# Kernel optimization log

Measured on AMD Instinct MI355X. Metric: run time of the kernel, lower is better.

## Reference

```python
import jax, jax.numpy as jnp
import numpy as np

N_SRC0, N_DST0 = 200000, 40000
N_SRC1, N_DST1 = 40000, 8000
E0, E1 = 1000000, 80000
D_IN, D_HID, D_OUT = 256, 512, 256


def setup_inputs() -> dict:
    key = jax.random.key(0)
    ks = jax.random.split(key, 10)
    return {
        "feat": jax.random.normal(ks[0], (N_SRC0, D_IN), dtype=jnp.float32),
        "Wself0": jax.random.normal(ks[1], (D_IN, D_HID), dtype=jnp.float32) * 0.05,
        "Wneigh0": jax.random.normal(ks[2], (D_IN, D_HID), dtype=jnp.float32) * 0.05,
        "b0": jnp.zeros((D_HID,), dtype=jnp.float32),
        "Wself1": jax.random.normal(ks[3], (D_HID, D_OUT), dtype=jnp.float32) * 0.05,
        "Wneigh1": jax.random.normal(ks[4], (D_HID, D_OUT), dtype=jnp.float32) * 0.05,
        "b1": jnp.zeros((D_OUT,), dtype=jnp.float32),
        "edge_src0": jax.random.randint(ks[5], (E0,), 0, N_SRC0, dtype=jnp.int32),
        "edge_dst0": jax.random.randint(ks[6], (E0,), 0, N_DST0, dtype=jnp.int32),
        "edge_src1": jax.random.randint(ks[7], (E1,), 0, N_SRC1, dtype=jnp.int32),
        "edge_dst1": jax.random.randint(ks[8], (E1,), 0, N_DST1, dtype=jnp.int32),
    }


def _mean_agg(h_src, src, dst, n_dst):
    # gather src features along edges, segment-mean over dst nodes
    msg_sum = jax.ops.segment_sum(h_src[src], dst, num_segments=n_dst)  # [n_dst, d]
    deg = jax.ops.segment_sum(jnp.ones(dst.shape, h_src.dtype), dst, num_segments=n_dst)
    return msg_sum / jnp.maximum(deg, 1.0)[:, None]


def _sage_layer(h, src, dst, n_dst, W_self, W_neigh, b):
    # DGL SAGEConv(mean): fc_self(h_dst) + fc_neigh(mean_neighbors) + bias
    h_dst = h[:n_dst]
    h_neigh = _mean_agg(h, src, dst, n_dst)
    return h_dst @ W_self + h_neigh @ W_neigh + b


def reference(feat, Wself0, Wneigh0, b0, Wself1, Wneigh1, b1,
              edge_src0, edge_dst0, edge_src1, edge_dst1):
    h = _sage_layer(feat, edge_src0, edge_dst0, N_DST0, Wself0, Wneigh0, b0)
    h = jax.nn.relu(h)  # ReLU between layers, not after last
    h = _sage_layer(h, edge_src1, edge_dst1, N_DST1, Wself1, Wneigh1, b1)
    return h
```

## Files before the change

### kernel.cpp

```cpp
#include <hip/hip_runtime.h>

#define DEV __device__ __forceinline__

typedef float f32x4 __attribute__((ext_vector_type(4)));
typedef short s16x4 __attribute__((ext_vector_type(4)));
typedef short s16x8 __attribute__((ext_vector_type(8)));

DEV float bf2f(short s) {
  unsigned u = ((unsigned)(unsigned short)s) << 16;
  return __builtin_bit_cast(float, u);
}
DEV short f2bf(float f) {
  unsigned u = __builtin_bit_cast(unsigned, f);
  u += 0x7FFFu + ((u >> 16) & 1u);
  return (short)(u >> 16);
}

DEV void gld_lds16(const void* g, void* l) {
  __builtin_amdgcn_global_load_lds(
      (const __attribute__((address_space(1))) void*)g,
      (__attribute__((address_space(3))) void*)l, 16, 0, 0);
}

__global__ void front_k(const float* __restrict__ feat, short* __restrict__ fbf, long nconv,
                        const float* __restrict__ Ws0, const float* __restrict__ Wn0,
                        short* __restrict__ W0T,
                        const float* __restrict__ Ws1, const float* __restrict__ Wn1,
                        short* __restrict__ W1T,
                        const int* __restrict__ es0, const int* __restrict__ ed0, int E0,
                        int* __restrict__ cnt0, int* __restrict__ bk0,
                        const int* __restrict__ es1, const int* __restrict__ ed1, int E1,
                        int* __restrict__ cnt1, int* __restrict__ bk1) {
  const int b = blockIdx.x, tid = threadIdx.x;
  if (b < 1664) {
    long i = ((long)b * 256 + tid) * 8;
    const long stride = (long)1664 * 256 * 8;
    for (; i < nconv; i += stride) {
      f32x4 v0 = *(const f32x4*)(feat + i);
      f32x4 v1 = *(const f32x4*)(feat + i + 4);
      s16x8 o;
      o[0] = f2bf(v0[0]); o[1] = f2bf(v0[1]); o[2] = f2bf(v0[2]); o[3] = f2bf(v0[3]);
      o[4] = f2bf(v1[0]); o[5] = f2bf(v1[1]); o[6] = f2bf(v1[2]); o[7] = f2bf(v1[3]);
      *(s16x8*)(fbf + i) = o;
    }
  } else if (b < 1728) {
    for (int idx = (b - 1664) * 256 + tid; idx < 524288; idx += 64 * 256) {
      if (idx < 262144) {
        int n = idx >> 9, k = idx & 511;
        float v = (k < 256) ? Ws0[(size_t)k * 512 + n] : Wn0[(size_t)(k - 256) * 512 + n];
        W0T[idx] = f2bf(v);
      } else {
        int i2 = idx - 262144;
        int n = i2 >> 10, k = i2 & 1023;
        float v = (k < 512) ? Ws1[(size_t)k * 256 + n] : Wn1[(size_t)(k - 512) * 256 + n];
        W1T[i2] = f2bf(v);
      }
    }
  } else if (b < 2016) {
    for (int e = (b - 1728) * 256 + tid; e < E0; e += 288 * 256) {
      int d = ed0[e];
      int p = atomicAdd(&cnt0[d], 1);
      if (p < 64) bk0[(d << 6) + p] = es0[e];
    }
  } else {
    for (int e = (b - 2016) * 256 + tid; e < E1; e += 32 * 256) {
      int d = ed1[e];
      int p = atomicAdd(&cnt1[d], 1);
      if (p < 48) bk1[d * 48 + p] = es1[e];
    }
  }
}

__global__ void agg_f32_256(const float* __restrict__ X, const int* __restrict__ cntA,
                            const int* __restrict__ bucket, short* __restrict__ out,
                            int n_dst) {
  int gw = (blockIdx.x * blockDim.x + threadIdx.x) >> 6;
  if (gw >= n_dst) return;
  int lane = threadIdx.x & 63;
  int start = gw << 6, cnt = cntA[gw];
  float a[4] = {0, 0, 0, 0}, b[4] = {0, 0, 0, 0};
  int i = 0;
  for (; i + 2 <= cnt; i += 2) {
    int s0 = bucket[start + i], s1 = bucket[start + i + 1];
    f32x4 v0 = *(const f32x4*)(X + (size_t)s0 * 256 + lane * 4);
    f32x4 v1 = *(const f32x4*)(X + (size_t)s1 * 256 + lane * 4);
#pragma unroll
    for (int j = 0; j < 4; ++j) { a[j] += v0[j]; b[j] += v1[j]; }
  }
  if (i < cnt) {
    int s0 = bucket[start + i];
    f32x4 v0 = *(const f32x4*)(X + (size_t)s0 * 256 + lane * 4);
#pragma unroll
    for (int j = 0; j < 4; ++j) a[j] += v0[j];
  }
  float inv = 1.0f / (float)(cnt > 0 ? cnt : 1);
  s16x4 o;
#pragma unroll
  for (int j = 0; j < 4; ++j) o[j] = f2bf((a[j] + b[j]) * inv);
  *(s16x4*)(out + (size_t)gw * 256 + lane * 4) = o;
}

__global__ void agg_bf16_256(const short* __restrict__ X, const int* __restrict__ cntA,
                             const int* __restrict__ bucket, short* __restrict__ out,
                             int n_dst) {
  int gw = (blockIdx.x * blockDim.x + threadIdx.x) >> 6;
  if (gw >= n_dst) return;
  int lane = threadIdx.x & 63;
  int half = lane >> 5;
  int cl = lane & 31;
  int start = gw << 6, cnt = cntA[gw];
  float a[8] = {0, 0, 0, 0, 0, 0, 0, 0}, b[8] = {0, 0, 0, 0, 0, 0, 0, 0};
  int i = 0;
  for (; i + 4 <= cnt; i += 4) {
    int s0 = bucket[start + i + half];
    int s1 = bucket[start + i + 2 + half];
    s16x8 v0 = *(const s16x8*)(X + (size_t)s0 * 256 + cl * 8);
    s16x8 v1 = *(const s16x8*)(X + (size_t)s1 * 256 + cl * 8);
#pragma unroll
    for (int j = 0; j < 8; ++j) { a[j] += bf2f(v0[j]); b[j] += bf2f(v1[j]); }
  }
  for (; i < cnt; i += 2) {
    int idx = i + half;
    if (idx < cnt) {
      int s0 = bucket[start + idx];
      s16x8 v0 = *(const s16x8*)(X + (size_t)s0 * 256 + cl * 8);
#pragma unroll
      for (int j = 0; j < 8; ++j) a[j] += bf2f(v0[j]);
    }
  }
  float inv = 1.0f / (float)(cnt > 0 ? cnt : 1);
  float r[8];
#pragma unroll
  for (int j = 0; j < 8; ++j) {
    float s = a[j] + b[j];
    r[j] = s + __shfl(s, lane ^ 32);
  }
  if (half == 0) {
    s16x8 o;
#pragma unroll
    for (int j = 0; j < 8; ++j) o[j] = f2bf(r[j] * inv);
    *(s16x8*)(out + (size_t)gw * 256 + cl * 8) = o;
  }
}

__global__ void agg_bf16_512(const short* __restrict__ X, const int* __restrict__ cntA,
                             const int* __restrict__ bucket, short* __restrict__ out,
                             int n_dst) {
  int gw = (blockIdx.x * blockDim.x + threadIdx.x) >> 6;
  if (gw >= n_dst) return;
  int lane = threadIdx.x & 63;
  int start = gw * 48, cnt = cntA[gw];
  float a[8] = {0, 0, 0, 0, 0, 0, 0, 0}, b[8] = {0, 0, 0, 0, 0, 0, 0, 0};
  float c[8] = {0, 0, 0, 0, 0, 0, 0, 0}, d[8] = {0, 0, 0, 0, 0, 0, 0, 0};
  int i = 0;
  for (; i + 4 <= cnt; i += 4) {
    int s0 = bucket[start + i], s1 = bucket[start + i + 1];
    int s2 = bucket[start + i + 2], s3 = bucket[start + i + 3];
    s16x8 v0 = *(const s16x8*)(X + (size_t)s0 * 512 + lane * 8);
    s16x8 v1 = *(const s16x8*)(X + (size_t)s1 * 512 + lane * 8);
    s16x8 v2 = *(const s16x8*)(X + (size_t)s2 * 512 + lane * 8);
    s16x8 v3 = *(const s16x8*)(X + (size_t)s3 * 512 + lane * 8);
#pragma unroll
    for (int j = 0; j < 8; ++j) {
      a[j] += bf2f(v0[j]); b[j] += bf2f(v1[j]);
      c[j] += bf2f(v2[j]); d[j] += bf2f(v3[j]);
    }
  }
  for (; i < cnt; ++i) {
    int s0 = bucket[start + i];
    s16x8 v0 = *(const s16x8*)(X + (size_t)s0 * 512 + lane * 8);
#pragma unroll
    for (int j = 0; j < 8; ++j) a[j] += bf2f(v0[j]);
  }
  float inv = 1.0f / (float)(cnt > 0 ? cnt : 1);
  s16x8 o;
#pragma unroll
  for (int j = 0; j < 8; ++j) o[j] = f2bf(((a[j] + b[j]) + (c[j] + d[j])) * inv);
  *(s16x8*)(out + (size_t)gw * 512 + lane * 8) = o;
}

template <int BM, int BN, bool RELU_BF16>
__global__ __launch_bounds__(256, 2) void gemm_k(
    const short* __restrict__ Aleft, const short* __restrict__ Aright,
    const short* __restrict__ Bt, const float* __restrict__ bias,
    void* __restrict__ Cout, int M, int N, int K, int KH) {
  constexpr int MFR = BM / 32;
  constexpr int NFR = BN / 32;
  constexpr int PA = BM / 32;
  constexpr int PB = BN / 32;
  __shared__ short As[BM * 64];
  __shared__ short Bs[BN * 64];
  const int tid = threadIdx.x;
  const int w = tid >> 6, lane = tid & 63;
  const int m0 = blockIdx.y * BM, n0 = blockIdx.x * BN;
  const int wr = w >> 1, wc = w & 1;
  const int lr = lane & 15, lk = (lane >> 4) << 3;

  f32x4 acc[MFR][NFR] = {};

  const int nkt = K >> 6;
  const int ktH = KH >> 6;
  const size_t ldA = (size_t)KH * 2;
  const size_t ldB = (size_t)K * 2;

  for (int kt = 0; kt < nkt; ++kt) {
    const char* Abase = (const char*)((kt < ktH) ? Aleft : Aright);
    const int ktl = (kt < ktH) ? kt : kt - ktH;
#pragma unroll
    for (int j = 0; j < PA; ++j) {
      int c = w * PA + j;
      int o = (c << 10) + lane * 16;
      int row = o >> 7;
      int kb = o & 127;
      int kbs = kb ^ ((row & 7) << 4);
      int ar = m0 + row; if (ar > M - 1) ar = M - 1;
      gld_lds16(Abase + (size_t)ar * ldA + (size_t)(ktl * 128 + kbs),
                ((char*)As) + (c << 10));
    }
#pragma unroll
    for (int j = 0; j < PB; ++j) {
      int c = w * PB + j;
      int o = (c << 10) + lane * 16;
      int row = o >> 7;
      int kb = o & 127;
      int kbs = kb ^ ((row & 7) << 4);
      gld_lds16((const char*)Bt + (size_t)(n0 + row) * ldB + (size_t)(kt * 128 + kbs),
                ((char*)Bs) + (c << 10));
    }
    __syncthreads();
#pragma unroll
    for (int kk = 0; kk < 2; ++kk) {
      s16x8 af[MFR], bfr[NFR];
      const int kbyte = (kk * 32 + lk) * 2;
#pragma unroll
      for (int m = 0; m < MFR; ++m) {
        int r = wr * (BM / 2) + m * 16 + lr;
        af[m] = *(const s16x8*)((const char*)As + (r << 7) + (kbyte ^ ((r & 7) << 4)));
      }
#pragma unroll
      for (int n = 0; n < NFR; ++n) {
        int r = wc * (BN / 2) + n * 16 + lr;
        bfr[n] = *(const s16x8*)((const char*)Bs + (r << 7) + (kbyte ^ ((r & 7) << 4)));
      }
#pragma unroll
      for (int m = 0; m < MFR; ++m)
#pragma unroll
        for (int n = 0; n < NFR; ++n)
          acc[m][n] = __builtin_amdgcn_mfma_f32_16x16x32_bf16(af[m], bfr[n], acc[m][n], 0, 0, 0);
    }
    __syncthreads();
  }

  const int rq = (lane >> 4) * 4;
#pragma unroll
  for (int m = 0; m < MFR; ++m) {
#pragma unroll
    for (int n = 0; n < NFR; ++n) {
      const int col = n0 + wc * (BN / 2) + n * 16 + lr;
      const float bv = bias[col];
#pragma unroll
      for (int j = 0; j < 4; ++j) {
        const int row = m0 + wr * (BM / 2) + m * 16 + rq + j;
        if (row < M) {
          float v = acc[m][n][j] + bv;
          if (RELU_BF16) {
            v = v > 0.0f ? v : 0.0f;
            ((short*)Cout)[(size_t)row * N + col] = f2bf(v);
          } else {
            ((float*)Cout)[(size_t)row * N + col] = v;
          }
        }
      }
    }
  }
}

extern "C" void kernel_launch(void* const* d_in, const int* in_sizes, int n_in,
                              void* d_out, int out_size, void* d_ws, size_t ws_size,
                              hipStream_t stream) {
  const int NS0 = 200000, ND0 = 40000, ND1 = 8000;
  const int E0 = 1000000, E1 = 80000;
  const int DIN = 256, DH = 512, DOUT = 256;

  const float* feat = (const float*)d_in[0];
  const float* Wself0 = (const float*)d_in[1];
  const float* Wneigh0 = (const float*)d_in[2];
  const float* b0 = (const float*)d_in[3];
  const float* Wself1 = (const float*)d_in[4];
  const float* Wneigh1 = (const float*)d_in[5];
  const float* b1 = (const float*)d_in[6];
  const int* es0 = (const int*)d_in[7];
  const int* ed0 = (const int*)d_in[8];
  const int* es1 = (const int*)d_in[9];
  const int* ed1 = (const int*)d_in[10];

  char* w = (char*)d_ws;
  size_t pos = 0;
  auto take = [&](size_t b) -> char* {
    char* p = w + pos;
    pos += (b + 255) & ~(size_t)255;
    return p;
  };

  short* hne0 = (short*)take((size_t)ND0 * DIN * 2);
  short* h = (short*)take((size_t)ND0 * DH * 2);
  short* hne1 = (short*)take((size_t)ND1 * DH * 2);
  short* hdst0buf = (short*)take((size_t)ND0 * DIN * 2);
  short* W0T = (short*)take((size_t)DH * 2 * DIN * 2);
  short* W1T = (short*)take((size_t)DOUT * 2 * DH * 2);
  int* cnt0 = (int*)take((size_t)ND0 * 4);
  int* cnt1 = (int*)take((size_t)ND1 * 4);
  int* bucket0 = (int*)take((size_t)ND0 * 64 * 4);
  int* bucket1 = (int*)take((size_t)ND1 * 48 * 4);
  short* featbf = (short*)take((size_t)NS0 * DIN * 2);
  const bool use_bf = (ws_size >= pos);
  (void)in_sizes; (void)n_in; (void)out_size;

  hipMemsetAsync(cnt0, 0, (size_t)(ND0 + ND1) * 4, stream);

  const short* hdst0 = use_bf ? featbf : hdst0buf;

  front_k<<<2048, 256, 0, stream>>>(
      feat, use_bf ? featbf : hdst0buf,
      use_bf ? (long)NS0 * DIN : (long)ND0 * DIN,
      Wself0, Wneigh0, W0T, Wself1, Wneigh1, W1T,
      es0, ed0, E0, cnt0, bucket0,
      es1, ed1, E1, cnt1, bucket1);

  if (use_bf)
    agg_bf16_256<<<ND0 / 4, 256, 0, stream>>>(featbf, cnt0, bucket0, hne0, ND0);
  else
    agg_f32_256<<<ND0 / 4, 256, 0, stream>>>(feat, cnt0, bucket0, hne0, ND0);

  gemm_k<128, 128, true><<<dim3(DH / 128, (ND0 + 127) / 128), 256, 0, stream>>>(
      hdst0, hne0, W0T, b0, h, ND0, DH, 2 * DIN, DIN);

  agg_bf16_512<<<ND1 / 4, 256, 0, stream>>>(h, cnt1, bucket1, hne1, ND1);

  gemm_k<64, 128, false><<<dim3(DOUT / 128, (ND1 + 63) / 64), 256, 0, stream>>>(
      h, hne1, W1T, b1, d_out, ND1, DOUT, 2 * DH, DH);
}
```

Baseline: 250.4 us.

## Bucket edges per destination range with LDS counters instead of global atomics

Edge bucketing now assigns each block a fixed range of 200 destination nodes. Every block scans the whole edge_dst array with vector loads and counts its own edges using shared-memory atomics, then writes the clamped counts back. This removes the global atomic contention and the memset of the count arrays. The cost is that every block rereads the entire edge array, which multiplies read traffic on the edge indices.

```diff
diff --git a/kernel.cpp b/kernel.cpp
--- a/kernel.cpp
+++ b/kernel.cpp
@@ -5,6 +5,7 @@
 typedef float f32x4 __attribute__((ext_vector_type(4)));
 typedef short s16x4 __attribute__((ext_vector_type(4)));
 typedef short s16x8 __attribute__((ext_vector_type(8)));
+typedef int i32x4 __attribute__((ext_vector_type(4)));
 
 DEV float bf2f(short s) {
   unsigned u = ((unsigned)(unsigned short)s) << 16;
@@ -31,6 +32,7 @@
                         int* __restrict__ cnt0, int* __restrict__ bk0,
                         const int* __restrict__ es1, const int* __restrict__ ed1, int E1,
                         int* __restrict__ cnt1, int* __restrict__ bk1) {
+  __shared__ int cnt_l[200];
   const int b = blockIdx.x, tid = threadIdx.x;
   if (b < 1664) {
     long i = ((long)b * 256 + tid) * 8;
@@ -56,18 +58,64 @@
         W1T[i2] = f2bf(v);
       }
     }
-  } else if (b < 2016) {
-    for (int e = (b - 1728) * 256 + tid; e < E0; e += 288 * 256) {
-      int d = ed0[e];
-      int p = atomicAdd(&cnt0[d], 1);
-      if (p < 64) bk0[(d << 6) + p] = es0[e];
-    }
+  } else if (b < 1928) {
+    const int lo = (b - 1728) * 200;
+    if (tid < 200) cnt_l[tid] = 0;
+    __syncthreads();
+    const i32x4* ed4 = (const i32x4*)ed0;
+    const int n4 = E0 >> 2;
+#pragma unroll 1
+    for (int i = tid * 2; i < n4; i += 512) {
+      i32x4 a = ed4[i];
+      i32x4 c = ed4[i + 1];
+#pragma unroll
+      for (int j = 0; j < 4; ++j) {
+        int d = a[j];
+        if ((unsigned)(d - lo) < 200u) {
+          int p = atomicAdd(&cnt_l[d - lo], 1);
+          if (p < 64) bk0[(d << 6) + p] = es0[4 * i + j];
+        }
+      }
+#pragma unroll
+      for (int j = 0; j < 4; ++j) {
+        int d = c[j];
+        if ((unsigned)(d - lo) < 200u) {
+          int p = atomicAdd(&cnt_l[d - lo], 1);
+          if (p < 64) bk0[(d << 6) + p] = es0[4 * (i + 1) + j];
+        }
+      }
+    }
+    __syncthreads();
+    if (tid < 200) cnt0[lo + tid] = min(cnt_l[tid], 64);
   } else {
-    for (int e = (b - 2016) * 256 + tid; e < E1; e += 32 * 256) {
-      int d = ed1[e];
-      int p = atomicAdd(&cnt1[d], 1);
-      if (p < 48) bk1[d * 48 + p] = es1[e];
-    }
+    const int lo = (b - 1928) * 200;
+    if (tid < 200) cnt_l[tid] = 0;
+    __syncthreads();
+    const i32x4* ed4 = (const i32x4*)ed1;
+    const int n4 = E1 >> 2;
+#pragma unroll 1
+    for (int i = tid * 2; i < n4; i += 512) {
+      i32x4 a = ed4[i];
+      i32x4 c = ed4[i + 1];
+#pragma unroll
+      for (int j = 0; j < 4; ++j) {
+        int d = a[j];
+        if ((unsigned)(d - lo) < 200u) {
+          int p = atomicAdd(&cnt_l[d - lo], 1);
+          if (p < 48) bk1[d * 48 + p] = es1[4 * i + j];
+        }
+      }
+#pragma unroll
+      for (int j = 0; j < 4; ++j) {
+        int d = c[j];
+        if ((unsigned)(d - lo) < 200u) {
+          int p = atomicAdd(&cnt_l[d - lo], 1);
+          if (p < 48) bk1[d * 48 + p] = es1[4 * (i + 1) + j];
+        }
+      }
+    }
+    __syncthreads();
+    if (tid < 200) cnt1[lo + tid] = min(cnt_l[tid], 48);
   }
 }
 
@@ -316,11 +364,9 @@
   const bool use_bf = (ws_size >= pos);
   (void)in_sizes; (void)n_in; (void)out_size;
 
-  hipMemsetAsync(cnt0, 0, (size_t)(ND0 + ND1) * 4, stream);
-
   const short* hdst0 = use_bf ? featbf : hdst0buf;
 
-  front_k<<<2048, 256, 0, stream>>>(
+  front_k<<<1968, 256, 0, stream>>>(
       feat, use_bf ? featbf : hdst0buf,
       use_bf ? (long)NS0 * DIN : (long)ND0 * DIN,
       Wself0, Wneigh0, W0T, Wself1, Wneigh1, W1T,
```

Measured after the change: 619.8 us. +147.6%, slower.
